# Optimization experiments

Hardware: AMD Instinct MI355X
Metric: run time of the kernel (lower is better)

The kernel has to match this reference:

```python
import jax, jax.numpy as jnp
import numpy as np

D_MODEL = 1024
N_HEADS = 16
HEAD_DIM = D_MODEL // N_HEADS


def setup_inputs() -> dict:
    key = jax.random.key(0)
    ks = jax.random.split(key, 5)
    s = 1.0 / np.sqrt(D_MODEL)
    return {
        "x": jax.random.normal(ks[0], (2, 2048, D_MODEL), dtype=jnp.float32),
        "w_qkv": jax.random.uniform(ks[1], (3 * D_MODEL, D_MODEL), jnp.float32, -s, s),
        "b_qkv": jax.random.uniform(ks[2], (3 * D_MODEL,), jnp.float32, -s, s),
        "w_out": jax.random.uniform(ks[3], (D_MODEL, D_MODEL), jnp.float32, -s, s),
        "b_out": jax.random.uniform(ks[4], (D_MODEL,), jnp.float32, -s, s),
    }


def _attn(x, w_qkv, b_qkv, w_out, b_out):
    bsz, seq_len, _ = x.shape
    qkv = jnp.einsum('bsd,ed->bse', x, w_qkv) + b_qkv  # [B,S,3D]
    q, k, v = jnp.split(qkv, 3, axis=-1)
    def heads(t):  # [B,S,D] -> [B,H,S,Dh]
        return t.reshape(bsz, seq_len, N_HEADS, HEAD_DIM).transpose(0, 2, 1, 3)
    q, k, v = heads(q), heads(k), heads(v)
    scores = jnp.einsum('bhqd,bhkd->bhqk', q, k) / np.sqrt(HEAD_DIM)
    mask = jnp.tril(jnp.ones((seq_len, seq_len), dtype=bool))
    scores = jnp.where(mask, scores, -jnp.inf)
    probs = jax.nn.softmax(scores, axis=-1)
    attn = jnp.einsum('bhqk,bhkd->bhqd', probs, v)
    attn = attn.transpose(0, 2, 1, 3).reshape(bsz, seq_len, D_MODEL)
    return jnp.einsum('bsd,ed->bse', attn, w_out) + b_out


def reference(x, w_qkv, b_qkv, w_out, b_out):
    return _attn(x, w_qkv, b_qkv, w_out, b_out)
```

## Files before the change

### kernel.cpp

```cpp
#include <hip/hip_runtime.h>
#include <hip/hip_bf16.h>
#include <stdint.h>

#define SEQ     2048
#define BATCH   2
#define NHEADS  16
#define HDIM    64
#define DMODEL  1024
#define N3      3072
#define D2      2048
#define MTOT    (BATCH*SEQ)

typedef __attribute__((ext_vector_type(4))) float f32x4;
typedef __attribute__((ext_vector_type(8))) short bf16x8;

static __device__ inline unsigned short f2bf(float f) {
    union { float f; unsigned u; } v; v.f = f;
    unsigned r = (v.u + 0x7fffu + ((v.u >> 16) & 1u)) >> 16;
    return (unsigned short)r;
}
static __device__ inline unsigned pk2bf(float a, float b) {
    union { __hip_bfloat162 h; unsigned u; } c;
    c.h = __float22bfloat162_rn(make_float2(a, b));
    return c.u;
}

#define GLDS(gp, lp) __builtin_amdgcn_global_load_lds( \
    (const __attribute__((address_space(1))) void*)(gp), \
    (__attribute__((address_space(3))) void*)(lp), 16, 0, 0)

__global__ void cast_all(const float* __restrict__ x,
                         const float* __restrict__ wqkv,
                         const float* __restrict__ wout,
                         unsigned short* __restrict__ xb,
                         unsigned short* __restrict__ wqkvb,
                         unsigned short* __restrict__ woutb) {
    long i4 = (long)(blockIdx.x * blockDim.x + threadIdx.x) * 4;
    const float* src; unsigned short* dst; long off;
    if (i4 < 4194304L)      { src = x;    dst = xb;    off = i4; }
    else if (i4 < 7340032L) { src = wqkv; dst = wqkvb; off = i4 - 4194304L; }
    else                    { src = wout; dst = woutb; off = i4 - 7340032L; }
    float4 v = *(const float4*)(src + off);
    union { uint2 u; ushort4 s; } pk;
    pk.u.x = pk2bf(v.x, v.y); pk.u.y = pk2bf(v.z, v.w);
    *(ushort4*)(dst + off) = pk.s;
}

__global__ __launch_bounds__(256, 2) void gemm_qkv(
    const unsigned short* __restrict__ A,
    const unsigned short* __restrict__ B,
    const float* __restrict__ bias,
    unsigned short* __restrict__ qk,
    unsigned short* __restrict__ vT)
{
    __shared__ __align__(16) unsigned short sA[2][128][64];
    __shared__ __align__(16) unsigned short sB[2][192][64];
    const int tid  = threadIdx.x;
    const int wave = tid >> 6, lane = tid & 63;
    const int quad = lane >> 4, l16 = lane & 15, l7 = l16 & 7;
    const int wm = wave >> 1, wn = wave & 1;
    const int m0 = blockIdx.x * 128, n0 = blockIdx.y * 192;

    f32x4 acc[4][6];
    const f32x4 zero = {0.f, 0.f, 0.f, 0.f};
    #pragma unroll
    for (int i = 0; i < 4; i++)
        #pragma unroll
        for (int j = 0; j < 6; j++) acc[i][j] = zero;

    const int rsel = tid >> 3;
    const int sgl  = (tid & 7) ^ (rsel & 7);
    const unsigned short* gA0 = A + (long)(m0 + rsel) * 1024 + sgl * 8;
    const unsigned short* gB0 = B + (long)(n0 + rsel) * 1024 + sgl * 8;

    #pragma unroll
    for (int i = 0; i < 4; i++)
        GLDS(gA0 + (long)(32 * i) * 1024, &sA[0][32 * i + wave * 8][0]);
    #pragma unroll
    for (int i = 0; i < 6; i++)
        GLDS(gB0 + (long)(32 * i) * 1024, &sB[0][32 * i + wave * 8][0]);

    int buf = 0;
    for (int k0 = 0; k0 < 1024; k0 += 64, buf ^= 1) {
        __syncthreads();
        if (k0 + 64 < 1024) {
            #pragma unroll
            for (int i = 0; i < 4; i++)
                GLDS(gA0 + (long)(32 * i) * 1024 + k0 + 64, &sA[buf ^ 1][32 * i + wave * 8][0]);
            #pragma unroll
            for (int i = 0; i < 6; i++)
                GLDS(gB0 + (long)(32 * i) * 1024 + k0 + 64, &sB[buf ^ 1][32 * i + wave * 8][0]);
        }
        #pragma unroll
        for (int ks = 0; ks < 2; ks++) {
            const int fseg = ((ks * 4 + quad) ^ l7) * 8;
            bf16x8 af[4], bfr[6];
            #pragma unroll
            for (int mt = 0; mt < 4; mt++)
                af[mt] = *(const bf16x8*)(&sA[buf][wm * 64 + mt * 16 + l16][fseg]);
            #pragma unroll
            for (int nt = 0; nt < 6; nt++)
                bfr[nt] = *(const bf16x8*)(&sB[buf][wn * 96 + nt * 16 + l16][fseg]);
            #pragma unroll
            for (int mt = 0; mt < 4; mt++)
                #pragma unroll
                for (int nt = 0; nt < 6; nt++)
                    acc[mt][nt] = __builtin_amdgcn_mfma_f32_16x16x32_bf16(
                        af[mt], bfr[nt], acc[mt][nt], 0, 0, 0);
        }
    }

    const int b = m0 >> 11;
    #pragma unroll
    for (int nt = 0; nt < 6; nt++) {
        const int n_g = n0 + wn * 96 + nt * 16 + l16;
        const float bv = bias[n_g];
        if (n_g < 2048) {
            #pragma unroll
            for (int mt = 0; mt < 4; mt++) {
                #pragma unroll
                for (int r = 0; r < 4; r++) {
                    const int m_g = m0 + wm * 64 + mt * 16 + quad * 4 + r;
                    qk[(long)m_g * D2 + n_g] = f2bf(acc[mt][nt][r] + bv);
                }
            }
        } else {
            const int dm = n_g - 2048;
            const long vrow = (long)(((b << 4) + (dm >> 6)) << 6) + (dm & 63);
            #pragma unroll
            for (int mt = 0; mt < 4; mt++) {
                const int m_g = m0 + wm * 64 + mt * 16 + quad * 4;
                union { uint2 u; ushort4 s; } pk;
                pk.u.x = pk2bf(acc[mt][nt][0] + bv, acc[mt][nt][1] + bv);
                pk.u.y = pk2bf(acc[mt][nt][2] + bv, acc[mt][nt][3] + bv);
                *(ushort4*)(vT + vrow * D2 + (m_g & 2047)) = pk.s;
            }
        }
    }
}

__global__ __launch_bounds__(256, 4) void gemm_out(
    const unsigned short* __restrict__ A,
    const unsigned short* __restrict__ B,
    const float* __restrict__ bias,
    float* __restrict__ C)
{
    __shared__ __align__(16) unsigned short sA[2][128][32];
    __shared__ __align__(16) unsigned short sB[2][64][32];
    const int tid  = threadIdx.x;
    const int wave = tid >> 6, lane = tid & 63;
    const int quad = lane >> 4, l16 = lane & 15;
    const int wm = wave >> 1, wn = wave & 1;
    const int m0 = blockIdx.x * 128, n0 = blockIdx.y * 64;

    f32x4 acc[4][2];
    const f32x4 zero = {0.f, 0.f, 0.f, 0.f};
    #pragma unroll
    for (int i = 0; i < 4; i++) { acc[i][0] = zero; acc[i][1] = zero; }

    const int rsel = tid >> 2;
    const int sgl  = (tid & 3) ^ ((tid >> 3) & 3);
    const unsigned short* gA0 = A + (long)(m0 + rsel) * 1024 + sgl * 8;
    const unsigned short* gB0 = B + (long)(n0 + rsel) * 1024 + sgl * 8;

    const int fs = (quad ^ ((l16 >> 1) & 3)) * 8;

    GLDS(gA0,              &sA[0][wave * 16][0]);
    GLDS(gA0 + 64L * 1024, &sA[0][64 + wave * 16][0]);
    GLDS(gB0,              &sB[0][wave * 16][0]);

    int buf = 0;
    for (int k0 = 0; k0 < 1024; k0 += 32, buf ^= 1) {
        __syncthreads();
        if (k0 + 32 < 1024) {
            GLDS(gA0 + k0 + 32,              &sA[buf ^ 1][wave * 16][0]);
            GLDS(gA0 + 64L * 1024 + k0 + 32, &sA[buf ^ 1][64 + wave * 16][0]);
            GLDS(gB0 + k0 + 32,              &sB[buf ^ 1][wave * 16][0]);
        }
        bf16x8 af[4], bfr[2];
        #pragma unroll
        for (int mt = 0; mt < 4; mt++)
            af[mt] = *(const bf16x8*)(&sA[buf][wm * 64 + mt * 16 + l16][fs]);
        #pragma unroll
        for (int nt = 0; nt < 2; nt++)
            bfr[nt] = *(const bf16x8*)(&sB[buf][wn * 32 + nt * 16 + l16][fs]);
        #pragma unroll
        for (int mt = 0; mt < 4; mt++)
            #pragma unroll
            for (int nt = 0; nt < 2; nt++)
                acc[mt][nt] = __builtin_amdgcn_mfma_f32_16x16x32_bf16(
                    af[mt], bfr[nt], acc[mt][nt], 0, 0, 0);
    }
    #pragma unroll
    for (int nt = 0; nt < 2; nt++) {
        const int n_g = n0 + wn * 32 + nt * 16 + l16;
        const float bv = bias[n_g];
        #pragma unroll
        for (int mt = 0; mt < 4; mt++) {
            #pragma unroll
            for (int r = 0; r < 4; r++) {
                const int m_g = m0 + wm * 64 + mt * 16 + quad * 4 + r;
                C[(long)m_g * DMODEL + n_g] = acc[mt][nt][r] + bv;
            }
        }
    }
}

__global__ __launch_bounds__(128) void attn_kernel(
    const unsigned short* __restrict__ qk,
    const unsigned short* __restrict__ vT,
    unsigned short* __restrict__ attn)
{
    __shared__ __align__(16) unsigned short sK [2][2][64][64];
    __shared__ __align__(16) unsigned short sVt[2][2][64][64];
    __shared__ __align__(16) unsigned short sP [2][2][16][64];

    const int tid  = threadIdx.x;
    const int w    = tid >> 6, lane = tid & 63;
    const int quad = lane >> 4, l16 = lane & 15, l7 = l16 & 7;

    const int bh = blockIdx.x;
    const int b  = bh >> 4, h = bh & 15;
    const int pair = blockIdx.y;
    const long rowb = (long)b * SEQ;

    const int rl = lane >> 3;
    const int sm = (lane & 7) ^ rl;
    const unsigned short* kg = qk + (rowb + w * 32 + rl) * D2 + 1024 + h * HDIM + sm * 8;
    const unsigned short* vg = vT + (long)(bh * 64 + w * 32 + rl) * D2 + sm * 8;

    const int s0 = quad ^ l7;
    const float C2 = 0.18033688011112042f;
    const f32x4 zero = {0.f, 0.f, 0.f, 0.f};

    #pragma unroll
    for (int ph = 0; ph < 2; ph++) {
        const int qtile  = ph ? (31 - pair) : pair;
        const int qbase  = qtile * 64;
        const int ntiles = qtile + 1;
        const int npairs = (ntiles + 1) >> 1;

        bf16x8 qfr[2][2];
        #pragma unroll
        for (int qf = 0; qf < 2; qf++) {
            const unsigned short* qp = qk + (rowb + qbase + w * 32 + qf * 16 + l16) * D2 + h * HDIM;
            qfr[qf][0] = *(const bf16x8*)(qp + quad * 8);
            qfr[qf][1] = *(const bf16x8*)(qp + 32 + quad * 8);
        }
        f32x4 Oacc[4][2];
        #pragma unroll
        for (int mf = 0; mf < 4; mf++) { Oacc[mf][0] = zero; Oacc[mf][1] = zero; }
        float l_i[2] = {0.f, 0.f};

        __syncthreads();
        {
            const int o0 = 0, o1 = (1 <= qtile ? 1 : qtile) * 64;
            #pragma unroll
            for (int i = 0; i < 4; i++) {
                GLDS(kg + (long)(o0 + 8 * i) * D2, &sK [0][0][w * 32 + 8 * i][0]);
                GLDS(vg + o0 + (long)(8 * i) * D2, &sVt[0][0][w * 32 + 8 * i][0]);
                GLDS(kg + (long)(o1 + 8 * i) * D2, &sK [0][1][w * 32 + 8 * i][0]);
                GLDS(vg + o1 + (long)(8 * i) * D2, &sVt[0][1][w * 32 + 8 * i][0]);
            }
        }

        int buf = 0;
        for (int p = 0; p < npairs; p++, buf ^= 1) {
            __syncthreads();
            if (p + 1 < npairs) {
                const int t0 = 2 * p + 2, t1 = 2 * p + 3;
                const int o0 = (t0 <= qtile ? t0 : qtile) * 64;
                const int o1 = (t1 <= qtile ? t1 : qtile) * 64;
                #pragma unroll
                for (int i = 0; i < 4; i++) {
                    GLDS(kg + (long)(o0 + 8 * i) * D2, &sK [buf ^ 1][0][w * 32 + 8 * i][0]);
                    GLDS(vg + o0 + (long)(8 * i) * D2, &sVt[buf ^ 1][0][w * 32 + 8 * i][0]);
                    GLDS(kg + (long)(o1 + 8 * i) * D2, &sK [buf ^ 1][1][w * 32 + 8 * i][0]);
                    GLDS(vg + o1 + (long)(8 * i) * D2, &sVt[buf ^ 1][1][w * 32 + 8 * i][0]);
                }
            }
            #pragma unroll
            for (int s = 0; s < 2; s++) {
                const int t = 2 * p + s;
                if (t >= ntiles) break;

                f32x4 st[4][2];
                #pragma unroll
                for (int kvf = 0; kvf < 4; kvf++) {
                    bf16x8 kf0 = *(const bf16x8*)(&sK[buf][s][kvf * 16 + l16][s0 * 8]);
                    bf16x8 kf1 = *(const bf16x8*)(&sK[buf][s][kvf * 16 + l16][(s0 ^ 4) * 8]);
                    #pragma unroll
                    for (int qf = 0; qf < 2; qf++) {
                        st[kvf][qf] = __builtin_amdgcn_mfma_f32_16x16x32_bf16(kf0, qfr[qf][0], zero, 0, 0, 0);
                        st[kvf][qf] = __builtin_amdgcn_mfma_f32_16x16x32_bf16(kf1, qfr[qf][1], st[kvf][qf], 0, 0, 0);
                    }
                }
                if (t == qtile) {
                    #pragma unroll
                    for (int qf = 0; qf < 2; qf++) {
                        const int ql = w * 32 + qf * 16 + l16;
                        #pragma unroll
                        for (int kvf = 0; kvf < 4; kvf++) {
                            const int kv = kvf * 16 + quad * 4;
                            #pragma unroll
                            for (int r = 0; r < 4; r++)
                                if (kv + r > ql) st[kvf][qf][r] = -1e30f;
                        }
                    }
                }
                #pragma unroll
                for (int qf = 0; qf < 2; qf++) {
                    #pragma unroll
                    for (int kvf = 0; kvf < 4; kvf++) {
                        #pragma unroll
                        for (int r = 0; r < 4; r++)
                            st[kvf][qf][r] = __builtin_amdgcn_exp2f(st[kvf][qf][r] * C2);
                    }
                    f32x4 ps = (st[0][qf] + st[1][qf]) + (st[2][qf] + st[3][qf]);
                    l_i[qf] += (ps[0] + ps[1]) + (ps[2] + ps[3]);
                    #pragma unroll
                    for (int kvf = 0; kvf < 4; kvf++) {
                        union { uint2 u; ushort4 s4; } pk;
                        pk.u.x = pk2bf(st[kvf][qf][0], st[kvf][qf][1]);
                        pk.u.y = pk2bf(st[kvf][qf][2], st[kvf][qf][3]);
                        const int seg = (kvf * 2 + (quad >> 1)) ^ l7;
                        *(ushort4*)(&sP[w][qf][l16][seg * 8 + (quad & 1) * 4]) = pk.s4;
                    }
                }
                bf16x8 pf[2][2];
                #pragma unroll
                for (int qf = 0; qf < 2; qf++) {
                    pf[qf][0] = *(const bf16x8*)(&sP[w][qf][l16][(quad ^ l7) * 8]);
                    pf[qf][1] = *(const bf16x8*)(&sP[w][qf][l16][((4 + quad) ^ l7) * 8]);
                }
                #pragma unroll
                for (int mf = 0; mf < 4; mf++) {
                    bf16x8 vf0 = *(const bf16x8*)(&sVt[buf][s][mf * 16 + l16][s0 * 8]);
                    bf16x8 vf1 = *(const bf16x8*)(&sVt[buf][s][mf * 16 + l16][(s0 ^ 4) * 8]);
                    #pragma unroll
                    for (int qf = 0; qf < 2; qf++) {
                        Oacc[mf][qf] = __builtin_amdgcn_mfma_f32_16x16x32_bf16(vf0, pf[qf][0], Oacc[mf][qf], 0, 0, 0);
                        Oacc[mf][qf] = __builtin_amdgcn_mfma_f32_16x16x32_bf16(vf1, pf[qf][1], Oacc[mf][qf], 0, 0, 0);
                    }
                }
            }
        }
        #pragma unroll
        for (int qf = 0; qf < 2; qf++) {
            float L = l_i[qf];
            L += __shfl_xor(L, 16);
            L += __shfl_xor(L, 32);
            const float inv = 1.0f / L;
            const int q = qbase + w * 32 + qf * 16 + l16;
            unsigned short* op = attn + (rowb + q) * DMODEL + h * HDIM + quad * 4;
            #pragma unroll
            for (int mf = 0; mf < 4; mf++) {
                union { uint2 u; ushort4 s4; } pk;
                pk.u.x = pk2bf(Oacc[mf][qf][0] * inv, Oacc[mf][qf][1] * inv);
                pk.u.y = pk2bf(Oacc[mf][qf][2] * inv, Oacc[mf][qf][3] * inv);
                *(ushort4*)(op + mf * 16) = pk.s4;
            }
        }
    }
}

extern "C" void kernel_launch(void* const* d_in, const int* in_sizes, int n_in,
                              void* d_out, int out_size, void* d_ws, size_t ws_size,
                              hipStream_t stream) {
    const float* x    = (const float*)d_in[0];
    const float* wqkv = (const float*)d_in[1];
    const float* bqkv = (const float*)d_in[2];
    const float* wout = (const float*)d_in[3];
    const float* bout = (const float*)d_in[4];

    char* ws = (char*)d_ws;
    unsigned short* xb    = (unsigned short*)(ws);
    unsigned short* wqkvb = (unsigned short*)(ws + (8L << 20));
    unsigned short* woutb = (unsigned short*)(ws + (14L << 20));
    unsigned short* qkb   = (unsigned short*)(ws + (16L << 20));
    unsigned short* vTb   = (unsigned short*)(ws + (32L << 20));
    unsigned short* attnb = (unsigned short*)(ws + (40L << 20));

    cast_all<<<8192, 256, 0, stream>>>(x, wqkv, wout, xb, wqkvb, woutb);

    dim3 g1(32, 16);
    gemm_qkv<<<g1, 256, 0, stream>>>(xb, wqkvb, bqkv, qkb, vTb);

    dim3 g2(32, 16);
    attn_kernel<<<g2, 128, 0, stream>>>(qkb, vTb, attnb);

    dim3 g3(32, 16);
    gemm_out<<<g3, 256, 0, stream>>>(attnb, woutb, bout, (float*)d_out);
}
```

Before: 178.1 us.

## Stage one KV tile per step instead of pairs to cut LDS and raise occupancy

```diff
diff --git a/kernel.cpp b/kernel.cpp
--- a/kernel.cpp
+++ b/kernel.cpp
@@ -206,13 +206,13 @@
     }
 }
 
-__global__ __launch_bounds__(128) void attn_kernel(
+__global__ __launch_bounds__(128, 2) void attn_kernel(
     const unsigned short* __restrict__ qk,
     const unsigned short* __restrict__ vT,
     unsigned short* __restrict__ attn)
 {
-    __shared__ __align__(16) unsigned short sK [2][2][64][64];
-    __shared__ __align__(16) unsigned short sVt[2][2][64][64];
+    __shared__ __align__(16) unsigned short sK [2][64][64];
+    __shared__ __align__(16) unsigned short sVt[2][64][64];
     __shared__ __align__(16) unsigned short sP [2][2][16][64];
 
     const int tid  = threadIdx.x;
@@ -238,7 +238,6 @@
         const int qtile  = ph ? (31 - pair) : pair;
         const int qbase  = qtile * 64;
         const int ntiles = qtile + 1;
-        const int npairs = (ntiles + 1) >> 1;
 
         bf16x8 qfr[2][2];
         #pragma unroll
@@ -253,95 +252,81 @@
         float l_i[2] = {0.f, 0.f};
 
         __syncthreads();
-        {
-            const int o0 = 0, o1 = (1 <= qtile ? 1 : qtile) * 64;
-            #pragma unroll
-            for (int i = 0; i < 4; i++) {
-                GLDS(kg + (long)(o0 + 8 * i) * D2, &sK [0][0][w * 32 + 8 * i][0]);
-                GLDS(vg + o0 + (long)(8 * i) * D2, &sVt[0][0][w * 32 + 8 * i][0]);
-                GLDS(kg + (long)(o1 + 8 * i) * D2, &sK [0][1][w * 32 + 8 * i][0]);
-                GLDS(vg + o1 + (long)(8 * i) * D2, &sVt[0][1][w * 32 + 8 * i][0]);
-            }
+        #pragma unroll
+        for (int i = 0; i < 4; i++) {
+            GLDS(kg + (long)(8 * i) * D2, &sK [0][w * 32 + 8 * i][0]);
+            GLDS(vg + (long)(8 * i) * D2, &sVt[0][w * 32 + 8 * i][0]);
         }
 
         int buf = 0;
-        for (int p = 0; p < npairs; p++, buf ^= 1) {
+        for (int t = 0; t < ntiles; ++t, buf ^= 1) {
             __syncthreads();
-            if (p + 1 < npairs) {
-                const int t0 = 2 * p + 2, t1 = 2 * p + 3;
-                const int o0 = (t0 <= qtile ? t0 : qtile) * 64;
-                const int o1 = (t1 <= qtile ? t1 : qtile) * 64;
+            if (t + 1 < ntiles) {
+                const int kvoff = (t + 1) * 64;
                 #pragma unroll
                 for (int i = 0; i < 4; i++) {
-                    GLDS(kg + (long)(o0 + 8 * i) * D2, &sK [buf ^ 1][0][w * 32 + 8 * i][0]);
-                    GLDS(vg + o0 + (long)(8 * i) * D2, &sVt[buf ^ 1][0][w * 32 + 8 * i][0]);
-                    GLDS(kg + (long)(o1 + 8 * i) * D2, &sK [buf ^ 1][1][w * 32 + 8 * i][0]);
-                    GLDS(vg + o1 + (long)(8 * i) * D2, &sVt[buf ^ 1][1][w * 32 + 8 * i][0]);
-                }
-            }
-            #pragma unroll
-            for (int s = 0; s < 2; s++) {
-                const int t = 2 * p + s;
-                if (t >= ntiles) break;
-
-                f32x4 st[4][2];
-                #pragma unroll
-                for (int kvf = 0; kvf < 4; kvf++) {
-                    bf16x8 kf0 = *(const bf16x8*)(&sK[buf][s][kvf * 16 + l16][s0 * 8]);
-                    bf16x8 kf1 = *(const bf16x8*)(&sK[buf][s][kvf * 16 + l16][(s0 ^ 4) * 8]);
-                    #pragma unroll
-                    for (int qf = 0; qf < 2; qf++) {
-                        st[kvf][qf] = __builtin_amdgcn_mfma_f32_16x16x32_bf16(kf0, qfr[qf][0], zero, 0, 0, 0);
-                        st[kvf][qf] = __builtin_amdgcn_mfma_f32_16x16x32_bf16(kf1, qfr[qf][1], st[kvf][qf], 0, 0, 0);
-                    }
-                }
-                if (t == qtile) {
-                    #pragma unroll
-                    for (int qf = 0; qf < 2; qf++) {
-                        const int ql = w * 32 + qf * 16 + l16;
-                        #pragma unroll
-                        for (int kvf = 0; kvf < 4; kvf++) {
-                            const int kv = kvf * 16 + quad * 4;
-                            #pragma unroll
-                            for (int r = 0; r < 4; r++)
-                                if (kv + r > ql) st[kvf][qf][r] = -1e30f;
-                        }
-                    }
-                }
+                    GLDS(kg + (long)(kvoff + 8 * i) * D2, &sK [buf ^ 1][w * 32 + 8 * i][0]);
+                    GLDS(vg + kvoff + (long)(8 * i) * D2, &sVt[buf ^ 1][w * 32 + 8 * i][0]);
+                }
+            }
+
+            f32x4 st[4][2];
+            #pragma unroll
+            for (int kvf = 0; kvf < 4; kvf++) {
+                bf16x8 kf0 = *(const bf16x8*)(&sK[buf][kvf * 16 + l16][s0 * 8]);
+                bf16x8 kf1 = *(const bf16x8*)(&sK[buf][kvf * 16 + l16][(s0 ^ 4) * 8]);
                 #pragma unroll
                 for (int qf = 0; qf < 2; qf++) {
+                    st[kvf][qf] = __builtin_amdgcn_mfma_f32_16x16x32_bf16(kf0, qfr[qf][0], zero, 0, 0, 0);
+                    st[kvf][qf] = __builtin_amdgcn_mfma_f32_16x16x32_bf16(kf1, qfr[qf][1], st[kvf][qf], 0, 0, 0);
+                }
+            }
+            if (t == qtile) {
+                #pragma unroll
+                for (int qf = 0; qf < 2; qf++) {
+                    const int ql = w * 32 + qf * 16 + l16;
                     #pragma unroll
                     for (int kvf = 0; kvf < 4; kvf++) {
+                        const int kv = kvf * 16 + quad * 4;
                         #pragma unroll
                         for (int r = 0; r < 4; r++)
-                            st[kvf][qf][r] = __builtin_amdgcn_exp2f(st[kvf][qf][r] * C2);
+                            if (kv + r > ql) st[kvf][qf][r] = -1e30f;
                     }
-                    f32x4 ps = (st[0][qf] + st[1][qf]) + (st[2][qf] + st[3][qf]);
-                    l_i[qf] += (ps[0] + ps[1]) + (ps[2] + ps[3]);
+                }
+            }
+            #pragma unroll
+            for (int qf = 0; qf < 2; qf++) {
+                #pragma unroll
+                for (int kvf = 0; kvf < 4; kvf++) {
                     #pragma unroll
-                    for (int kvf = 0; kvf < 4; kvf++) {
-                        union { uint2 u; ushort4 s4; } pk;
-                        pk.u.x = pk2bf(st[kvf][qf][0], st[kvf][qf][1]);
-                        pk.u.y = pk2bf(st[kvf][qf][2], st[kvf][qf][3]);
-                        const int seg = (kvf * 2 + (quad >> 1)) ^ l7;
-                        *(ushort4*)(&sP[w][qf][l16][seg * 8 + (quad & 1) * 4]) = pk.s4;
-                    }
-                }
-                bf16x8 pf[2][2];
+                    for (int r = 0; r < 4; r++)
+                        st[kvf][qf][r] = __builtin_amdgcn_exp2f(st[kvf][qf][r] * C2);
+                }
+                f32x4 ps = (st[0][qf] + st[1][qf]) + (st[2][qf] + st[3][qf]);
+                l_i[qf] += (ps[0] + ps[1]) + (ps[2] + ps[3]);
+                #pragma unroll
+                for (int kvf = 0; kvf < 4; kvf++) {
+                    union { uint2 u; ushort4 s4; } pk;
+                    pk.u.x = pk2bf(st[kvf][qf][0], st[kvf][qf][1]);
+                    pk.u.y = pk2bf(st[kvf][qf][2], st[kvf][qf][3]);
+                    const int seg = (kvf * 2 + (quad >> 1)) ^ l7;
+                    *(ushort4*)(&sP[w][qf][l16][seg * 8 + (quad & 1) * 4]) = pk.s4;
+                }
+            }
+            bf16x8 pf[2][2];
+            #pragma unroll
+            for (int qf = 0; qf < 2; qf++) {
+                pf[qf][0] = *(const bf16x8*)(&sP[w][qf][l16][(quad ^ l7) * 8]);
+                pf[qf][1] = *(const bf16x8*)(&sP[w][qf][l16][((4 + quad) ^ l7) * 8]);
+            }
+            #pragma unroll
+            for (int mf = 0; mf < 4; mf++) {
+                bf16x8 vf0 = *(const bf16x8*)(&sVt[buf][mf * 16 + l16][s0 * 8]);
+                bf16x8 vf1 = *(const bf16x8*)(&sVt[buf][mf * 16 + l16][(s0 ^ 4) * 8]);
                 #pragma unroll
                 for (int qf = 0; qf < 2; qf++) {
-                    pf[qf][0] = *(const bf16x8*)(&sP[w][qf][l16][(quad ^ l7) * 8]);
-                    pf[qf][1] = *(const bf16x8*)(&sP[w][qf][l16][((4 + quad) ^ l7) * 8]);
-                }
-                #pragma unroll
-                for (int mf = 0; mf < 4; mf++) {
-                    bf16x8 vf0 = *(const bf16x8*)(&sVt[buf][s][mf * 16 + l16][s0 * 8]);
-                    bf16x8 vf1 = *(const bf16x8*)(&sVt[buf][s][mf * 16 + l16][(s0 ^ 4) * 8]);
-                    #pragma unroll
-                    for (int qf = 0; qf < 2; qf++) {
-                        Oacc[mf][qf] = __builtin_amdgcn_mfma_f32_16x16x32_bf16(vf0, pf[qf][0], Oacc[mf][qf], 0, 0, 0);
-                        Oacc[mf][qf] = __builtin_amdgcn_mfma_f32_16x16x32_bf16(vf1, pf[qf][1], Oacc[mf][qf], 0, 0, 0);
-                    }
+                    Oacc[mf][qf] = __builtin_amdgcn_mfma_f32_16x16x32_bf16(vf0, pf[qf][0], Oacc[mf][qf], 0, 0, 0);
+                    Oacc[mf][qf] = __builtin_amdgcn_mfma_f32_16x16x32_bf16(vf1, pf[qf][1], Oacc[mf][qf], 0, 0, 0);
                 }
             }
         }
```

Result: slower. 183.0 us (+2.7%).
